# Performance work log

Hardware: AMD Instinct MI355X
Metric: run time of the kernel (lower is better)

The kernel has to match this reference:

```python
import jax, jax.numpy as jnp
import numpy as np

L1 = 1536
L2 = 15
L3 = 64
COUNT = 8
B = 16384


def setup_inputs() -> dict:
    key = jax.random.key(0)
    ks = jax.random.split(key, 10)
    d_in = 2 * L1 // 2  # 1536
    s1 = 1.0 / np.sqrt(d_in)
    s2 = 1.0 / np.sqrt(2 * L2)
    s3 = 1.0 / np.sqrt(L3)
    return {
        "x": jax.random.normal(ks[0], (B, d_in), dtype=jnp.float32),
        "ls_indices": jax.random.randint(ks[1], (B,), 0, COUNT, dtype=jnp.int32),
        "W1": jax.random.uniform(ks[2], (COUNT * (L2 + 1), d_in), jnp.float32, -s1, s1),
        "b1": jax.random.uniform(ks[3], (COUNT * (L2 + 1),), jnp.float32, -s1, s1),
        "Wf": jax.random.uniform(ks[4], (L2 + 1, d_in), jnp.float32, -s1, s1),
        "bf": jax.random.uniform(ks[5], (L2 + 1,), jnp.float32, -s1, s1),
        "W2": jax.random.uniform(ks[6], (COUNT * L3, 2 * L2), jnp.float32, -s2, s2),
        "b2": jax.random.uniform(ks[7], (COUNT * L3,), jnp.float32, -s2, s2),
        "Wo": jax.random.uniform(ks[8], (COUNT, L3), jnp.float32, -s3, s3),
        "bo": jax.random.uniform(ks[9], (COUNT,), jnp.float32, -s3, s3),
    }


def reference(x, ls_indices, W1, b1, Wf, bf, W2, b2, Wo, bo):
    count = Wo.shape[0]
    n = x.shape[0]
    idx = ls_indices[:, None, None]  # [B,1,1] selects the per-sample stack

    # l1: all stacks, then gather selected stack row per sample
    l1s = (x @ W1.T + b1).reshape(n, count, L2 + 1)          # [B, count, 16]
    l1f = x @ Wf.T + bf                                       # [B, 16]
    l1c = jnp.take_along_axis(l1s, idx, axis=1)[:, 0]         # [B, 16]

    l1c_, l1c_out = l1c[:, :L2], l1c[:, L2:]                  # [B,15], [B,1]
    l1f_, l1f_out = l1f[:, :L2], l1f[:, L2:]
    l1x = l1c_ + l1f_
    # squared-clipped-ReLU concat: [pow(x,2)*127/128, x] clamped to [0,1]
    l1x = jnp.clip(jnp.concatenate([l1x * l1x * (127.0 / 128.0), l1x], axis=1), 0.0, 1.0)  # [B,30]

    l2s = (l1x @ W2.T + b2).reshape(n, count, L3)             # [B, count, 64]
    l2c = jnp.take_along_axis(l2s, idx, axis=1)[:, 0]         # [B, 64]
    l2x = jnp.clip(l2c, 0.0, 1.0)

    l3s = (l2x @ Wo.T + bo).reshape(n, count, 1)              # [B, count, 1]
    l3c = jnp.take_along_axis(l3s, idx, axis=1)[:, 0]         # [B, 1]
    return l3c + l1f_out + l1c_out
```

## Files before the change

kernel.cpp:

```cpp
#include <hip/hip_runtime.h>
#include <hip/hip_bf16.h>
#include <stdint.h>

#define L1DIM 1536
#define NOUT  144
#define MTILE 16
#define NITER 12

#define W2L_OFF 528
#define WOL_OFF 8240
#define B2L_OFF 8776
#define B1L_OFF 9312
#define BFL_OFF 9448
#define SMW     9464

typedef __bf16 bf16;
typedef __bf16 bf16x8 __attribute__((ext_vector_type(8)));
typedef float  floatx4 __attribute__((ext_vector_type(4)));

__global__ __launch_bounds__(256) void pack_weights(
    const float* __restrict__ W1, const float* __restrict__ Wf,
    bf16* __restrict__ pw)
{
    int t = blockIdx.x * 256 + threadIdx.x;
    int n = t / 192;
    int o = t % 192;
    const float* src = (n < 128) ? (W1 + (size_t)n * L1DIM + o * 8)
                                 : (Wf + (size_t)(n - 128) * L1DIM + o * 8);
    float4 s0 = ((const float4*)src)[0];
    float4 s1 = ((const float4*)src)[1];
    bf16x8 v;
    v[0] = (bf16)s0.x; v[1] = (bf16)s0.y; v[2] = (bf16)s0.z; v[3] = (bf16)s0.w;
    v[4] = (bf16)s1.x; v[5] = (bf16)s1.y; v[6] = (bf16)s1.z; v[7] = (bf16)s1.w;
    *(bf16x8*)(pw + ((size_t)o * NOUT + n) * 8) = v;
}

__device__ __forceinline__ bf16x8 cvt8(float4 a, float4 b) {
    bf16x8 r;
    r[0] = (bf16)a.x; r[1] = (bf16)a.y; r[2] = (bf16)a.z; r[3] = (bf16)a.w;
    r[4] = (bf16)b.x; r[5] = (bf16)b.y; r[6] = (bf16)b.z; r[7] = (bf16)b.w;
    return r;
}

__device__ __forceinline__ uint32_t pk_bf16(float a, float b) {
    union { __bf16 h[2]; uint32_t u; } r;
    r.h[0] = (__bf16)a; r.h[1] = (__bf16)b;
    return r.u;
}

__global__ __launch_bounds__(256, 4) void layerstacks_main(
    const float* __restrict__ x, const int* __restrict__ lsidx,
    const bf16* __restrict__ pw,
    const float* __restrict__ b1, const float* __restrict__ bf_,
    const float* __restrict__ W2, const float* __restrict__ b2,
    const float* __restrict__ Wo, const float* __restrict__ bo,
    float* __restrict__ out)
{
    __shared__ uint32_t smu[SMW];
    float* sm = (float*)smu;

    const int tid  = threadIdx.x;
    const int wv   = tid >> 6;
    const int ln   = tid & 63;
    const int quad = ln >> 4;
    const int lm   = ln & 15;

    const int R0 = blockIdx.x * MTILE;

    const float* ax = x + (size_t)(R0 + lm) * L1DIM + wv * 384 + quad * 8;

    floatx4 acc[9];
#pragma unroll
    for (int i = 0; i < 9; i++) acc[i] = (floatx4){0.f, 0.f, 0.f, 0.f};

#pragma unroll
    for (int ki = 0; ki < NITER; ki++) {
        float4 a0 = *(const float4*)(ax + ki * 32);
        float4 a1 = *(const float4*)(ax + ki * 32 + 4);
        const bf16* bsl = pw + (size_t)(wv * 48 + ki * 4 + quad) * (NOUT * 8);
        bf16x8 af = cvt8(a0, a1);
#pragma unroll
        for (int t = 0; t < 9; t++) {
            bf16x8 bfr = *(const bf16x8*)(bsl + (size_t)(t * 16 + lm) * 8);
            acc[t] = __builtin_amdgcn_mfma_f32_16x16x32_bf16(af, bfr, acc[t], 0, 0, 0);
        }
    }

#pragma unroll
    for (int r = 0; r < 4; r++) {
        const int row = quad * 4 + r;
        const int bkt = lsidx[R0 + row];
        float c = acc[0][r];
#pragma unroll
        for (int t = 1; t < 8; t++) c = (bkt == t) ? acc[t][r] : c;
        sm[wv * 528 + row * 33 + lm]      = c;
        sm[wv * 528 + row * 33 + 16 + lm] = acc[8][r];
    }
    __syncthreads();

    {
        const int col = tid & 31;
        const int rr  = tid >> 5;
#pragma unroll
        for (int p = 0; p < 2; p++) {
            const int row = rr + p * 8;
            sm[row * 33 + col] = sm[row * 33 + col] + sm[528 + row * 33 + col]
                               + sm[1056 + row * 33 + col] + sm[1584 + row * 33 + col];
        }
    }
    __syncthreads();

    for (int w = tid; w < 7680; w += 256) {
        const int oi = w / 15, j = w % 15;
        float2 s = *(const float2*)(W2 + (size_t)oi * 30 + 2 * j);
        smu[W2L_OFF + (oi >> 6) * 964 + (oi & 63) * 15 + j] = pk_bf16(s.x, s.y);
    }
    for (int i = tid; i < 512; i += 256) {
        const int b = i >> 6, loc = i & 63;
        sm[WOL_OFF + b * 67 + loc] = Wo[i];
        sm[B2L_OFF + b * 67 + loc] = b2[i];
    }
    if (tid < 128) sm[B1L_OFF + (tid >> 4) * 17 + (tid & 15)] = b1[tid];
    if (tid < 16)  sm[BFL_OFF + tid] = bf_[tid];
    __syncthreads();

    {
        const int er   = tid >> 4;
        const int s16  = tid & 15;
        const int grow = R0 + er;
        const int bkt  = lsidx[grow];

        const float* b1r = &sm[B1L_OFF + bkt * 17];
        const float l1c15 = sm[er * 33 + 15] + b1r[15];
        const float l1f15 = sm[er * 33 + 31] + sm[BFL_OFF + 15];

        float l1x[30];
#pragma unroll
        for (int j = 0; j < 15; j++) {
            float tj = (sm[er * 33 + j] + b1r[j])
                     + (sm[er * 33 + 16 + j] + sm[BFL_OFF + j]);
            float sq = tj * tj * (127.0f / 128.0f);
            l1x[j]      = fminf(fmaxf(sq, 0.f), 1.f);
            l1x[15 + j] = fminf(fmaxf(tj, 0.f), 1.f);
        }

        float part = 0.f;
#pragma unroll
        for (int o = 0; o < 4; o++) {
            const int loc = s16 + 16 * o;
            const uint32_t* wrow = &smu[W2L_OFF + bkt * 964 + loc * 15];
            float a = sm[B2L_OFF + bkt * 67 + loc];
#pragma unroll
            for (int j = 0; j < 15; j++) {
                union { uint32_t u; __bf16 h[2]; } c;
                c.u = wrow[j];
                a += l1x[2 * j] * (float)c.h[0] + l1x[2 * j + 1] * (float)c.h[1];
            }
            a = fminf(fmaxf(a, 0.f), 1.f);
            part += a * sm[WOL_OFF + bkt * 67 + loc];
        }
        part += __shfl_xor(part, 1);
        part += __shfl_xor(part, 2);
        part += __shfl_xor(part, 4);
        part += __shfl_xor(part, 8);
        if (s16 == 0) out[grow] = part + bo[bkt] + l1c15 + l1f15;
    }
}

extern "C" void kernel_launch(void* const* d_in, const int* in_sizes, int n_in,
                              void* d_out, int out_size, void* d_ws, size_t ws_size,
                              hipStream_t stream) {
    const float* x   = (const float*)d_in[0];
    const int*   idx = (const int*)  d_in[1];
    const float* W1  = (const float*)d_in[2];
    const float* b1  = (const float*)d_in[3];
    const float* Wf  = (const float*)d_in[4];
    const float* bf  = (const float*)d_in[5];
    const float* W2  = (const float*)d_in[6];
    const float* b2  = (const float*)d_in[7];
    const float* Wo  = (const float*)d_in[8];
    const float* bo  = (const float*)d_in[9];
    float* out = (float*)d_out;
    bf16*  pw  = (bf16*)d_ws;

    pack_weights<<<dim3(108), dim3(256), 0, stream>>>(W1, Wf, pw);
    layerstacks_main<<<dim3(16384 / MTILE), dim3(256), 0, stream>>>(
        x, idx, pw, b1, bf, W2, b2, Wo, bo, out);
}
```

Baseline: 189.1 us.

## Sort rows by bucket within windows and skip MFMAs for absent stacks

Each block now takes a 128-row window, ranks the rows by stack index in shared memory, and handles one 16-row slice of that sorted order. A wave-uniform bitmask of the buckets present in the slice lets the layer-1 loop skip the weight loads and MFMAs for stacks that none of its rows use, which cuts matrix work and weight traffic. In exchange, every block redoes the 128-element rank sort, adds several barriers, and gathers x rows through a permutation. Since x reads likely dominate, the saving in MFMA work may be small.

```diff
diff --git a/kernel.cpp b/kernel.cpp
--- a/kernel.cpp
+++ b/kernel.cpp
@@ -6,13 +6,16 @@
 #define NOUT  144
 #define MTILE 16
 #define NITER 12
+#define WIN   128
 
 #define W2L_OFF 528
 #define WOL_OFF 8240
 #define B2L_OFF 8776
 #define B1L_OFF 9312
 #define BFL_OFF 9448
-#define SMW     9464
+#define SKY_OFF 9464
+#define SPM_OFF 9592
+#define SMW     9720
 
 typedef __bf16 bf16;
 typedef __bf16 bf16x8 __attribute__((ext_vector_type(8)));
@@ -57,7 +60,9 @@
     float* __restrict__ out)
 {
     __shared__ uint32_t smu[SMW];
-    float* sm = (float*)smu;
+    float* sm    = (float*)smu;
+    int*   skeys = (int*)&smu[SKY_OFF];
+    int*   sperm = (int*)&smu[SPM_OFF];
 
     const int tid  = threadIdx.x;
     const int wv   = tid >> 6;
@@ -65,9 +70,34 @@
     const int quad = ln >> 4;
     const int lm   = ln & 15;
 
-    const int R0 = blockIdx.x * MTILE;
-
-    const float* ax = x + (size_t)(R0 + lm) * L1DIM + wv * 384 + quad * 8;
+    const int win   = blockIdx.x >> 3;
+    const int slice = blockIdx.x & 7;
+    const int base  = win * WIN;
+
+    if (tid < WIN) skeys[tid] = lsidx[base + tid];
+    __syncthreads();
+
+    if (tid < WIN) {
+        const int key = skeys[tid];
+        int rank = 0;
+        for (int j = 0; j < WIN; j++) {
+            const int kj = skeys[j];
+            rank += (kj < key) | ((kj == key) & (j < tid));
+        }
+        sperm[rank] = base + tid;
+    }
+    __syncthreads();
+    if (tid < WIN) skeys[tid] = lsidx[sperm[tid]];
+    __syncthreads();
+
+    int nm = 0;
+#pragma unroll
+    for (int r = 0; r < 16; r++) nm |= 1 << skeys[slice * 16 + r];
+    nm = __builtin_amdgcn_readfirstlane(nm);
+
+    const int myrow = sperm[slice * 16 + lm];
+
+    const float* ax = x + (size_t)myrow * L1DIM + wv * 384 + quad * 8;
 
     floatx4 acc[9];
 #pragma unroll
@@ -81,15 +111,17 @@
         bf16x8 af = cvt8(a0, a1);
 #pragma unroll
         for (int t = 0; t < 9; t++) {
-            bf16x8 bfr = *(const bf16x8*)(bsl + (size_t)(t * 16 + lm) * 8);
-            acc[t] = __builtin_amdgcn_mfma_f32_16x16x32_bf16(af, bfr, acc[t], 0, 0, 0);
+            if (t == 8 || ((nm >> t) & 1)) {
+                bf16x8 bfr = *(const bf16x8*)(bsl + (size_t)(t * 16 + lm) * 8);
+                acc[t] = __builtin_amdgcn_mfma_f32_16x16x32_bf16(af, bfr, acc[t], 0, 0, 0);
+            }
         }
     }
 
 #pragma unroll
     for (int r = 0; r < 4; r++) {
         const int row = quad * 4 + r;
-        const int bkt = lsidx[R0 + row];
+        const int bkt = skeys[slice * 16 + row];
         float c = acc[0][r];
 #pragma unroll
         for (int t = 1; t < 8; t++) c = (bkt == t) ? acc[t][r] : c;
@@ -127,8 +159,8 @@
     {
         const int er   = tid >> 4;
         const int s16  = tid & 15;
-        const int grow = R0 + er;
-        const int bkt  = lsidx[grow];
+        const int grow = sperm[slice * 16 + er];
+        const int bkt  = skeys[slice * 16 + er];
 
         const float* b1r = &sm[B1L_OFF + bkt * 17];
         const float l1c15 = sm[er * 33 + 15] + b1r[15];
```

Result: faster. 184.9 us (-2.2%).
